# Optimization experiments

Hardware: AMD Instinct MI355X
Metric: run time of the kernel (lower is better)

The kernel has to match this reference:

```python
import jax, jax.numpy as jnp
from jax import lax
import numpy as np

S, B, HP, WP, CIN, CO, DS, DI, K = 6, 1, 37, 37, 1536, 256, 16, 512, 4
N = HP * WP          # 1369 patches (37x37 grid)
OH, OW = 148, 148
HID = max(S * CO // 4, S)  # 384, attention hidden


def setup_inputs() -> dict:
    key = jax.random.key(0)
    ks = iter(jax.random.split(key, 64))
    def nrm(shape, scale):
        return jax.random.normal(next(ks), shape, jnp.float32) * scale
    inp = {}
    inp["features"] = nrm((S, B, 1, N, CIN), 1.0)
    # AdaptiveFusionModule (global branch)
    inp["proj_w"] = nrm((S, CO, CIN), CIN ** -0.5)          # per-source 1x1 conv
    inp["attn_w1"] = nrm((S * CO, HID), (S * CO) ** -0.5)
    inp["attn_b1"] = jnp.zeros((HID,), jnp.float32)
    inp["attn_w2"] = nrm((HID, S), HID ** -0.5)
    inp["attn_b2"] = jnp.zeros((S,), jnp.float32)
    inp["src_scale"] = jnp.ones((S,), jnp.float32)
    # two SelectiveSSM parameter sets (fwd / bwd scan)
    def ssm_params(tag):
        d = {}
        d[tag + "_in_w"] = nrm((CO, 2 * DI), CO ** -0.5)
        d[tag + "_conv_w"] = nrm((K, DI), K ** -0.5)         # depthwise causal conv
        d[tag + "_conv_b"] = jnp.zeros((DI,), jnp.float32)
        d[tag + "_xp_w"] = nrm((DI, 2 * DS + DI + 1), 0.02)  # B, C, delta, dt_bias
        # trained A_log; scaled so the log-domain cumsum stays in fp32 range over L=1369
        d[tag + "_Alog"] = jnp.log(jnp.arange(1, DS + 1, dtype=jnp.float32) / 1000.0) * jnp.ones((DI, 1), jnp.float32)
        d[tag + "_D"] = jnp.ones((DI,), jnp.float32)
        d[tag + "_out_w"] = nrm((DI, CO), DI ** -0.5)
        d[tag + "_ln_g"] = jnp.ones((CO,), jnp.float32)
        d[tag + "_ln_b"] = jnp.zeros((CO,), jnp.float32)
        return d
    inp.update(ssm_params("f"))
    inp.update(ssm_params("b"))
    inp["merge_w"] = nrm((2 * CO, CO), (2 * CO) ** -0.5)     # MSSR merge 1x1 conv
    inp["co1_w"] = nrm((3, 3, CO, CO), (9 * CO) ** -0.5)     # conv_out1, HWIO
    inp["co1_b"] = jnp.zeros((CO,), jnp.float32)
    inp["hp"], inp["wp"], inp["out_h"], inp["out_w"] = HP, WP, OH, OW
    return inp


def _causal_dwconv(z, w, b):
    # z: [B,L,D], w: [K,D] -> torch Conv1d(groups=D, padding=K-1)[..., :L]
    Kk, L = w.shape[0], z.shape[1]
    zp = jnp.pad(z, ((0, 0), (Kk - 1, 0), (0, 0)))
    return sum(zp[:, k:k + L, :] * w[k] for k in range(Kk)) + b


def _ssm(x, in_w, conv_w, conv_b, xp_w, Alog, D, out_w, ln_g, ln_b):
    # x: [B,L,d_model] -> [B,L,d_model]
    z, gate = jnp.split(x @ in_w, 2, axis=-1)               # [B,L,DI] each
    z = jax.nn.silu(_causal_dwconv(z, conv_w, conv_b))
    xp = z @ xp_w                                           # [B,L,2*DS+DI+1]
    ds = Alog.shape[1]
    Bp, Cp = xp[..., :ds], xp[..., ds:2 * ds]
    delta = jax.nn.softplus(xp[..., 2 * ds:-1] + xp[..., -1:])  # [B,L,DI]
    dA = jnp.exp(delta[..., None] * (-jnp.exp(Alog)))       # [B,L,DI,DS]
    dBu = delta[..., None] * Bp[:, :, None, :] * z[..., None]
    # log-domain cumsum scan: h[t] = sum_s exp(cs[t]-cs[s]) * dBu[s]
    cs = jnp.cumsum(jnp.log(jnp.clip(dA, 1e-38)), axis=1)
    h = jnp.exp(cs) * jnp.cumsum(jnp.exp(-cs) * dBu, axis=1)
    y = (h * Cp[:, :, None, :]).sum(-1) + D * z             # [B,L,DI]
    y = (y * jax.nn.silu(gate)) @ out_w                     # [B,L,d_model]
    r = y + x                                               # residual + LayerNorm
    mu = r.mean(-1, keepdims=True)
    v = ((r - mu) ** 2).mean(-1, keepdims=True)
    return ln_g * (r - mu) * lax.rsqrt(v + 1e-5) + ln_b


def _forward(features, proj_w, attn_w1, attn_b1, attn_w2, attn_b2, src_scale,
             f_in_w, f_conv_w, f_conv_b, f_xp_w, f_Alog, f_D, f_out_w, f_ln_g, f_ln_b,
             b_in_w, b_conv_w, b_conv_b, b_xp_w, b_Alog, b_D, b_out_w, b_ln_g, b_ln_b,
             merge_w, co1_w, co1_b, hp, wp, out_h, out_w):
    feats = features[:, :, 0]                               # [S,B,N,Cin]
    pf = jnp.einsum('sbnc,soc->sbno', feats, proj_w)        # [S,B,N,Co] per-source 1x1 proj
    Bsz = pf.shape[1]
    concat = pf.mean(2).transpose(1, 0, 2).reshape(Bsz, -1)  # [B,S*Co] pooled concat
    w = jax.nn.softmax(jax.nn.relu(concat @ attn_w1 + attn_b1) @ attn_w2 + attn_b2, axis=-1)
    w = jax.nn.softmax(w * src_scale, axis=-1)              # double softmax as in torch
    fused = jnp.einsum('bs,sbnc->bnc', w, pf)               # [B,N,Co]
    # MSSR bidirectional scan over row-major flattened patches
    fwd = _ssm(fused, f_in_w, f_conv_w, f_conv_b, f_xp_w, f_Alog, f_D, f_out_w, f_ln_g, f_ln_b)
    bwd = _ssm(fused[:, ::-1], b_in_w, b_conv_w, b_conv_b, b_xp_w, b_Alog, b_D, b_out_w, b_ln_g, b_ln_b)[:, ::-1]
    out = jnp.concatenate([fwd, bwd], axis=-1) @ merge_w    # [B,N,Co]
    sp = out.reshape(Bsz, hp, wp, -1)                       # NHWC
    up = jax.image.resize(sp, (Bsz, out_h, out_w, sp.shape[-1]), method='bilinear')
    y = lax.conv_general_dilated(up, co1_w, (1, 1), 'SAME',
                                 dimension_numbers=('NHWC', 'HWIO', 'NHWC')) + co1_b
    return y.transpose(0, 3, 1, 2)                          # [B,Co,out_h,out_w]


def reference(features, proj_w, attn_w1, attn_b1, attn_w2, attn_b2, src_scale,
              f_in_w, f_conv_w, f_conv_b, f_xp_w, f_Alog, f_D, f_out_w, f_ln_g, f_ln_b,
              b_in_w, b_conv_w, b_conv_b, b_xp_w, b_Alog, b_D, b_out_w, b_ln_g, b_ln_b,
              merge_w, co1_w, co1_b, hp, wp, out_h, out_w):
    return _forward(features, proj_w, attn_w1, attn_b1, attn_w2, attn_b2, src_scale,
                    f_in_w, f_conv_w, f_conv_b, f_xp_w, f_Alog, f_D, f_out_w, f_ln_g, f_ln_b,
                    b_in_w, b_conv_w, b_conv_b, b_xp_w, b_Alog, b_D, b_out_w, b_ln_g, b_ln_b,
                    merge_w, co1_w, co1_b, hp, wp, out_h, out_w)
```

## Files before the change

kernel.cpp:

```cpp
#include <hip/hip_runtime.h>
#include <math.h>


namespace {
constexpr int kS   = 6;
constexpr int kHP  = 37;
constexpr int kWP  = 37;
constexpr int kN   = 1369;
constexpr int kCIN = 1536;
constexpr int kCO  = 256;
constexpr int kDS  = 16;
constexpr int kDI  = 512;
constexpr int kHID = 384;
constexpr int kOH  = 148;
constexpr int kOW  = 148;
constexpr int kNP  = kOH * kOW;
constexpr int kXPW = 545;
constexpr long kXPS = 746112;
constexpr int kNC  = 24;
constexpr int kCH  = 58;

constexpr long OFF_PF      = 0;
constexpr long OFF_Z2B     = 0;
constexpr long OFF_YGB     = 0;
constexpr long OFF_UPB     = 0;
constexpr long OFF_SCANP   = 700928;
constexpr long OFF_SCANH   = 1094144;
constexpr long OFF_HIN     = 1487360;
constexpr long OFF_OUTWT   = 1880576;
constexpr long OFF_COLPART = 2102784;
constexpr long OFF_WFIN    = 2119680;
constexpr long OFF_ATTNP   = 2119696;
constexpr long OFF_INWT    = 2200000;
constexpr long OFF_FUSEDB  = 2462144;
constexpr long OFF_ZG      = 2820624;
constexpr long OFF_Z       = 5760000;
constexpr long OFF_WCONVB  = 6000000;
constexpr long OFF_XP      = 7161856;
constexpr long OFF_DELTA   = 8654080;
constexpr long OFF_Y       = 10055936;
constexpr long OFF_GT      = 11457792;
constexpr long OFF_XPWT    = 11457792;
constexpr long OFF_FUSED2  = 12158720;
constexpr long OFF_CAT     = 12859648;
constexpr long OFF_MERGEWT = 13210112;
constexpr long OFF_MERGED  = 13560576;
}

typedef __attribute__((ext_vector_type(8))) short bf16x8;
typedef __attribute__((ext_vector_type(4))) float f32x4;

__device__ __forceinline__ short f2bf(float x) {
    unsigned u = __builtin_bit_cast(unsigned, x);
    unsigned r = u + 0x7fffu + ((u >> 16) & 1u);
    return (short)(r >> 16);
}

__device__ __forceinline__ bf16x8 cvt8(float4 x, float4 y) {
    union { short s[8]; bf16x8 v; } u;
    u.s[0] = f2bf(x.x); u.s[1] = f2bf(x.y); u.s[2] = f2bf(x.z); u.s[3] = f2bf(x.w);
    u.s[4] = f2bf(y.x); u.s[5] = f2bf(y.y); u.s[6] = f2bf(y.z); u.s[7] = f2bf(y.w);
    return u.v;
}

__global__ __launch_bounds__(256)
void transpose_cast_kernel(const float* __restrict__ w0, const float* __restrict__ w1,
                           short* __restrict__ wt, int K, int N)
{
    __shared__ float tile[32][33];
    int dir = blockIdx.z;
    const float* w = dir ? w1 : w0;
    short* o = wt + (long)dir * K * N;
    int k0 = blockIdx.x * 32, n0 = blockIdx.y * 32;
    int tx = threadIdx.x & 31, ty = threadIdx.x >> 5;
    #pragma unroll
    for (int r = 0; r < 32; r += 8) {
        int k = k0 + ty + r, n = n0 + tx;
        tile[ty + r][tx] = (k < K && n < N) ? w[(long)k * N + n] : 0.f;
    }
    __syncthreads();
    #pragma unroll
    for (int r = 0; r < 32; r += 8) {
        int n = n0 + ty + r, k = k0 + tx;
        if (n < N && k < K) o[(long)n * K + k] = f2bf(tile[tx][ty + r]);
    }
}

__global__ __launch_bounds__(256)
void mfma_nt(const short* __restrict__ A, long sA,
             const short* __restrict__ B, long sB,
             float* __restrict__ C, long sC,
             int M, int N, int K)
{
    __shared__ short smem[2][4096];
    const int bz = blockIdx.z;
    const short* Ab = A + (long)bz * sA;
    const short* Bb = B + (long)bz * sB;
    float* Cb = C + (long)bz * sC;
    const int t = threadIdx.x, w = t >> 6, l = t & 63;
    const int lr = l & 15, sg = l >> 4;
    const int m0 = blockIdx.x * 64, n0 = blockIdx.y * 64;

    const int row = t >> 2, qa = t & 3;
    int am = m0 + row; if (am >= M) am = M - 1;
    int bn = n0 + row; if (bn >= N) bn = N - 1;
    const long ga = (long)am * K + qa * 8;
    const long gb = (long)bn * K + qa * 8;
    const int woffA = row * 64 + ((qa ^ ((row >> 1) & 3)) << 4);
    const int woffB = 4096 + woffA;

    int aoff[2], boff[2];
    #pragma unroll
    for (int mi = 0; mi < 2; ++mi) {
        int r = (w >> 1) * 32 + mi * 16 + lr;
        aoff[mi] = r * 64 + ((sg ^ ((r >> 1) & 3)) << 4);
    }
    #pragma unroll
    for (int ni = 0; ni < 2; ++ni) {
        int r = (w & 1) * 32 + ni * 16 + lr;
        boff[ni] = 4096 + r * 64 + ((sg ^ ((r >> 1) & 3)) << 4);
    }

    f32x4 acc[2][2] = {};
    const int NT = K >> 5;
    {
        bf16x8 sa = *(const bf16x8*)(Ab + ga);
        bf16x8 sb = *(const bf16x8*)(Bb + gb);
        char* lb = (char*)&smem[0][0];
        *(bf16x8*)(lb + woffA) = sa;
        *(bf16x8*)(lb + woffB) = sb;
    }
    __syncthreads();
    for (int tt = 0; tt < NT; ++tt) {
        bf16x8 nsa, nsb;
        if (tt + 1 < NT) {
            long o = (long)(tt + 1) * 32;
            nsa = *(const bf16x8*)(Ab + ga + o);
            nsb = *(const bf16x8*)(Bb + gb + o);
        }
        char* lb = (char*)&smem[tt & 1][0];
        bf16x8 a[2], b[2];
        #pragma unroll
        for (int mi = 0; mi < 2; ++mi) a[mi] = *(const bf16x8*)(lb + aoff[mi]);
        #pragma unroll
        for (int ni = 0; ni < 2; ++ni) b[ni] = *(const bf16x8*)(lb + boff[ni]);
        #pragma unroll
        for (int mi = 0; mi < 2; ++mi)
            #pragma unroll
            for (int ni = 0; ni < 2; ++ni)
                acc[mi][ni] = __builtin_amdgcn_mfma_f32_16x16x32_bf16(a[mi], b[ni], acc[mi][ni], 0, 0, 0);
        if (tt + 1 < NT) {
            char* nb = (char*)&smem[(tt + 1) & 1][0];
            *(bf16x8*)(nb + woffA) = nsa;
            *(bf16x8*)(nb + woffB) = nsb;
        }
        __syncthreads();
    }
    const int q = l >> 4;
    const int wm0 = m0 + (w >> 1) * 32, wn0 = n0 + (w & 1) * 32;
    #pragma unroll
    for (int mi = 0; mi < 2; ++mi)
        #pragma unroll
        for (int ni = 0; ni < 2; ++ni)
            #pragma unroll
            for (int r = 0; r < 4; ++r) {
                int m = wm0 + mi * 16 + q * 4 + r;
                int n = wn0 + ni * 16 + lr;
                if (m < M && n < N)
                    Cb[(long)m * N + n] = acc[mi][ni][r];
            }
}

__global__ __launch_bounds__(256)
void proj_mfma_kernel(const float* __restrict__ Af, const float* __restrict__ Bf,
                      float* __restrict__ pf)
{
    __shared__ short smem[2][10240];
    const int bid = blockIdx.x;
    const int xcd = bid & 7, slot = bid >> 3;
    const int wid = (xcd < 4) ? xcd * 17 + slot : 68 + (xcd - 4) * 16 + slot;
    const int s = wid / 22, mblk = wid - s * 22;
    const float* A = Af + (long)s * kN * kCIN;
    const float* B = Bf + (long)s * kCO * kCIN;
    float* C = pf + (long)s * kN * kCO;
    const int m0 = mblk * 64;

    const int t = threadIdx.x, w = t >> 6, l = t & 63;
    const int lr = l & 15, sg = l >> 4;

    const int row = t >> 2, qa = t & 3;
    int am = m0 + row; if (am >= kN) am = kN - 1;
    const long ga = (long)am * kCIN + qa * 8;
    const int woffA = row * 64 + ((qa ^ ((row >> 1) & 3)) << 4);
    long gb[4]; int woffB[4];
    #pragma unroll
    for (int j = 0; j < 4; ++j) {
        int br = row + j * 64;
        gb[j] = (long)br * kCIN + qa * 8;
        woffB[j] = 4096 + br * 64 + ((qa ^ ((br >> 1) & 3)) << 4);
    }

    int aoff[4], boff[4];
    #pragma unroll
    for (int mi = 0; mi < 4; ++mi) {
        int r = mi * 16 + lr;
        aoff[mi] = r * 64 + ((sg ^ ((r >> 1) & 3)) << 4);
    }
    #pragma unroll
    for (int ni = 0; ni < 4; ++ni) {
        int r = w * 64 + ni * 16 + lr;
        boff[ni] = 4096 + r * 64 + ((sg ^ ((r >> 1) & 3)) << 4);
    }

    f32x4 acc[4][4] = {};
    const int NT = kCIN >> 5;
    {
        char* lb = (char*)&smem[0][0];
        float4 a0 = *(const float4*)(A + ga), a1 = *(const float4*)(A + ga + 4);
        *(bf16x8*)(lb + woffA) = cvt8(a0, a1);
        #pragma unroll
        for (int j = 0; j < 4; ++j) {
            float4 b0 = *(const float4*)(B + gb[j]), b1 = *(const float4*)(B + gb[j] + 4);
            *(bf16x8*)(lb + woffB[j]) = cvt8(b0, b1);
        }
    }
    __syncthreads();
    for (int tt = 0; tt < NT; ++tt) {
        float4 na0, na1, nb0[4], nb1[4];
        if (tt + 1 < NT) {
            long o = (long)(tt + 1) * 32;
            na0 = *(const float4*)(A + ga + o);
            na1 = *(const float4*)(A + ga + o + 4);
            #pragma unroll
            for (int j = 0; j < 4; ++j) {
                nb0[j] = *(const float4*)(B + gb[j] + o);
                nb1[j] = *(const float4*)(B + gb[j] + o + 4);
            }
        }
        char* lb = (char*)&smem[tt & 1][0];
        bf16x8 a[4], b[4];
        #pragma unroll
        for (int mi = 0; mi < 4; ++mi) a[mi] = *(const bf16x8*)(lb + aoff[mi]);
        #pragma unroll
        for (int ni = 0; ni < 4; ++ni) b[ni] = *(const bf16x8*)(lb + boff[ni]);
        #pragma unroll
        for (int mi = 0; mi < 4; ++mi)
            #pragma unroll
            for (int ni = 0; ni < 4; ++ni)
                acc[mi][ni] = __builtin_amdgcn_mfma_f32_16x16x32_bf16(a[mi], b[ni], acc[mi][ni], 0, 0, 0);
        if (tt + 1 < NT) {
            char* nb = (char*)&smem[(tt + 1) & 1][0];
            *(bf16x8*)(nb + woffA) = cvt8(na0, na1);
            #pragma unroll
            for (int j = 0; j < 4; ++j)
                *(bf16x8*)(nb + woffB[j]) = cvt8(nb0[j], nb1[j]);
        }
        __syncthreads();
    }
    const int q = l >> 4;
    const int wn0 = w * 64;
    #pragma unroll
    for (int mi = 0; mi < 4; ++mi)
        #pragma unroll
        for (int ni = 0; ni < 4; ++ni)
            #pragma unroll
            for (int r = 0; r < 4; ++r) {
                int m = m0 + mi * 16 + q * 4 + r;
                if (m < kN)
                    C[(long)m * kCO + wn0 + ni * 16 + lr] = acc[mi][ni][r];
            }
}

__global__ __launch_bounds__(256)
void conv_mfma_kernel(const short* __restrict__ up, const short* __restrict__ wt,
                      const float* __restrict__ bias, float* __restrict__ out)
{
    __shared__ short smem[2][12288];
    const int t = threadIdx.x, w = t >> 6, l = t & 63;
    const int lr = l & 15, sg = l >> 4;
    const int pm0 = blockIdx.x * 64;
    const int bn0 = blockIdx.y * 128;

    const int srow = t >> 3, qa = t & 7;
    long gA[2]; int woffA[2];
    #pragma unroll
    for (int j = 0; j < 2; ++j) {
        int ar = srow + j * 32;
        int p = pm0 + ar; if (p >= kNP) p = kNP - 1;
        int oy = p / kOW, ox = p - oy * kOW;
        gA[j] = ((long)oy * 150 + ox) * kCO + qa * 8;
        woffA[j] = ar * 128 + ((qa ^ (ar & 7)) << 4);
    }
    long gB[4]; int woffB[4];
    #pragma unroll
    for (int j = 0; j < 4; ++j) {
        int br = srow + j * 32;
        gB[j] = (long)(bn0 + br) * 2304 + qa * 8;
        woffB[j] = 8192 + br * 128 + ((qa ^ (br & 7)) << 4);
    }

    int aoff[2][2], boff[4][2];
    #pragma unroll
    for (int mi = 0; mi < 2; ++mi) {
        int r = (w >> 1) * 32 + mi * 16 + lr;
        #pragma unroll
        for (int kk = 0; kk < 2; ++kk)
            aoff[mi][kk] = r * 128 + (((kk * 4 + sg) ^ (r & 7)) << 4);
    }
    #pragma unroll
    for (int ni = 0; ni < 4; ++ni) {
        int r = (w & 1) * 64 + ni * 16 + lr;
        #pragma unroll
        for (int kk = 0; kk < 2; ++kk)
            boff[ni][kk] = 8192 + r * 128 + (((kk * 4 + sg) ^ (r & 7)) << 4);
    }

    f32x4 acc[2][4] = {};
    const int NT = 36;
    {
        char* lb = (char*)&smem[0][0];
        #pragma unroll
        for (int j = 0; j < 2; ++j)
            *(bf16x8*)(lb + woffA[j]) = *(const bf16x8*)(up + gA[j]);
        #pragma unroll
        for (int j = 0; j < 4; ++j)
            *(bf16x8*)(lb + woffB[j]) = *(const bf16x8*)(wt + gB[j]);
    }
    __syncthreads();

    for (int tt = 0; tt < NT; ++tt) {
        bf16x8 sa[2], sb[4];
        if (tt + 1 < NT) {
            int tn = tt + 1;
            int tap = tn >> 2, c0 = (tn & 3) << 6;
            int ky = tap / 3, kx = tap - ky * 3;
            long ta = ((long)ky * 150 + kx) * kCO + c0;
            long tb = (long)tn * 64;
            #pragma unroll
            for (int j = 0; j < 2; ++j) sa[j] = *(const bf16x8*)(up + gA[j] + ta);
            #pragma unroll
            for (int j = 0; j < 4; ++j) sb[j] = *(const bf16x8*)(wt + gB[j] + tb);
        }
        char* lb = (char*)&smem[tt & 1][0];
        #pragma unroll
        for (int kk = 0; kk < 2; ++kk) {
            bf16x8 a[2], b[4];
            #pragma unroll
            for (int mi = 0; mi < 2; ++mi) a[mi] = *(const bf16x8*)(lb + aoff[mi][kk]);
            #pragma unroll
            for (int ni = 0; ni < 4; ++ni) b[ni] = *(const bf16x8*)(lb + boff[ni][kk]);
            #pragma unroll
            for (int mi = 0; mi < 2; ++mi)
                #pragma unroll
                for (int ni = 0; ni < 4; ++ni)
                    acc[mi][ni] = __builtin_amdgcn_mfma_f32_16x16x32_bf16(a[mi], b[ni], acc[mi][ni], 0, 0, 0);
        }
        if (tt + 1 < NT) {
            char* nb = (char*)&smem[(tt + 1) & 1][0];
            #pragma unroll
            for (int j = 0; j < 2; ++j) *(bf16x8*)(nb + woffA[j]) = sa[j];
            #pragma unroll
            for (int j = 0; j < 4; ++j) *(bf16x8*)(nb + woffB[j]) = sb[j];
        }
        __syncthreads();
    }

    const int q = l >> 4;
    const int m0 = pm0 + (w >> 1) * 32;
    const int n0 = bn0 + (w & 1) * 64;
    #pragma unroll
    for (int mi = 0; mi < 2; ++mi)
        #pragma unroll
        for (int ni = 0; ni < 4; ++ni) {
            const int co = n0 + ni * 16 + lr;
            const float bv = bias[co];
            #pragma unroll
            for (int r = 0; r < 4; ++r) {
                int p = m0 + mi * 16 + q * 4 + r;
                if (p < kNP)
                    out[(long)co * kNP + p] = acc[mi][ni][r] + bv;
            }
        }
}

__global__ __launch_bounds__(256)
void colmean_kernel(const float* __restrict__ pf, float* __restrict__ colpart)
{
    int s = blockIdx.x, ch = blockIdx.y, o = threadIdx.x;
    int n0 = ch * 128, n1 = n0 + 128 > kN ? kN : n0 + 128;
    float a = 0.f;
    for (int n = n0; n < n1; ++n) a += pf[((long)s * kN + n) * kCO + o];
    colpart[ch * kS * kCO + s * kCO + o] = a;
}

__global__ __launch_bounds__(384)
void attn_part1(const float* __restrict__ colpart, const float* __restrict__ w1,
                float* __restrict__ partial)
{
    __shared__ float cm[128];
    int b = blockIdx.x, t = threadIdx.x;
    int c0 = b * 128;
    if (t < 128) {
        float a = 0.f;
        #pragma unroll
        for (int ch = 0; ch < 11; ++ch) a += colpart[ch * kS * kCO + c0 + t];
        cm[t] = a * (1.f / kN);
    }
    __syncthreads();
    float acc = 0.f;
    #pragma unroll 4
    for (int c = 0; c < 128; ++c) acc += cm[c] * w1[(long)(c0 + c) * kHID + t];
    partial[b * kHID + t] = acc;
}

__global__ __launch_bounds__(384)
void attn_part2(const float* __restrict__ partial, const float* __restrict__ b1,
                const float* __restrict__ w2, const float* __restrict__ b2,
                const float* __restrict__ ss, float* __restrict__ wfin)
{
    __shared__ float h[kHID];
    __shared__ float logits[8];
    int t = threadIdx.x;
    float acc = b1[t];
    #pragma unroll
    for (int b = 0; b < 12; ++b) acc += partial[b * kHID + t];
    h[t] = fmaxf(acc, 0.f);
    __syncthreads();
    if (t < kS) {
        float lg = b2[t];
        for (int j = 0; j < kHID; ++j) lg += h[j] * w2[j * kS + t];
        logits[t] = lg;
    }
    __syncthreads();
    if (t == 0) {
        float w[kS], mx = -1e30f, sum = 0.f;
        for (int s = 0; s < kS; ++s) mx = fmaxf(mx, logits[s]);
        for (int s = 0; s < kS; ++s) { w[s] = expf(logits[s] - mx); sum += w[s]; }
        for (int s = 0; s < kS; ++s) w[s] /= sum;
        mx = -1e30f;
        for (int s = 0; s < kS; ++s) { w[s] *= ss[s]; mx = fmaxf(mx, w[s]); }
        sum = 0.f;
        float e[kS];
        for (int s = 0; s < kS; ++s) { e[s] = expf(w[s] - mx); sum += e[s]; }
        for (int s = 0; s < kS; ++s) wfin[s] = e[s] / sum;
    }
}

__global__ __launch_bounds__(256)
void fuse_kernel(const float* __restrict__ pf, const float* __restrict__ wfin,
                 float* __restrict__ fused2, short* __restrict__ fusedb2)
{
    long idx = (long)blockIdx.x * 256 + threadIdx.x;
    if (idx >= (long)kN * kCO) return;
    float acc = 0.f;
    #pragma unroll
    for (int s = 0; s < kS; ++s) acc += wfin[s] * pf[(long)s * kN * kCO + idx];
    long n = idx / kCO; int c = (int)(idx % kCO);
    long ridx = (long)kN * kCO + (kN - 1 - n) * kCO + c;
    short bv = f2bf(acc);
    fused2[idx] = acc;
    fused2[ridx] = acc;
    fusedb2[idx] = bv;
    fusedb2[ridx] = bv;
}

__global__ __launch_bounds__(256)
void dwconv_kernel(const float* __restrict__ zg2,
                   const float* __restrict__ wf, const float* __restrict__ bf,
                   const float* __restrict__ wb, const float* __restrict__ bb,
                   float* __restrict__ z2, short* __restrict__ z2b)
{
    long idx = (long)blockIdx.x * 256 + threadIdx.x;
    int dir = blockIdx.y;
    if (idx >= (long)kN * kDI) return;
    long n = idx >> 9; int i = (int)(idx & (kDI - 1));
    const float* zg = zg2 + (long)dir * kN * 2 * kDI;
    const float* w  = dir ? wb : wf;
    const float* b  = dir ? bb : bf;
    float acc = b[i];
    #pragma unroll
    for (int k = 0; k < 4; ++k) {
        long m = n - 3 + k;
        if (m >= 0) acc += w[k * kDI + i] * zg[m * 2 * kDI + i];
    }
    float sg = 1.f / (1.f + expf(-acc));
    float v = acc * sg;
    z2 [(long)dir * kN * kDI + idx] = v;
    z2b[(long)dir * kN * kDI + idx] = f2bf(v);
}

__global__ __launch_bounds__(256)
void delta_kernel(const float* __restrict__ xp2, float* __restrict__ delta2)
{
    long idx = (long)blockIdx.x * 256 + threadIdx.x;
    int dir = blockIdx.y;
    if (idx >= (long)kN * kDI) return;
    long n = idx >> 9; int i = (int)(idx & (kDI - 1));
    const float* xp = xp2 + (long)dir * kXPS + n * kXPW;
    float x = xp[2 * kDS + i] + xp[kXPW - 1];
    float sp = fmaxf(x, 0.f) + log1pf(expf(-fabsf(x)));
    delta2[(long)dir * kN * kDI + idx] = sp;
}

__global__ __launch_bounds__(256)
void scan_partA(const float* __restrict__ delta2, const float* __restrict__ z2,
                const float* __restrict__ xp2,
                const float* __restrict__ Alogf, const float* __restrict__ Alogb,
                float* __restrict__ chunkP, float* __restrict__ chunkH)
{
    int bx = blockIdx.x;
    int c  = blockIdx.y;
    int dir = bx >> 5, iblk = bx & 31;
    int t = threadIdx.x;
    int s = t & 15, il = t >> 4;
    int i = iblk * 16 + il;
    int gid = dir * 8192 + iblk * 256 + t;
    const float* delta = delta2 + (long)dir * kN * kDI;
    const float* z     = z2     + (long)dir * kN * kDI;
    const float* xp    = xp2    + (long)dir * kXPS;
    const float* Alog  = dir ? Alogb : Alogf;
    float A = expf(Alog[i * kDS + s]);
    int n0 = c * kCH, n1 = n0 + kCH; if (n1 > kN) n1 = kN;
    float h = 0.f, P = 1.f;
    for (int n = n0; n < n1; ++n) {
        float dlt = delta[(long)n * kDI + i];
        float zv  = z[(long)n * kDI + i];
        float Bv  = xp[(long)n * kXPW + s];
        float dA  = __expf(-dlt * A);
        h = dA * h + dlt * Bv * zv;
        P *= dA;
    }
    chunkP[(long)c * 16384 + gid] = P;
    chunkH[(long)c * 16384 + gid] = h;
}

__global__ __launch_bounds__(256)
void scan_partB(const float* __restrict__ chunkP, const float* __restrict__ chunkH,
                float* __restrict__ hin)
{
    int gid = blockIdx.x * 256 + threadIdx.x;
    float H = 0.f;
    for (int c = 0; c < kNC; ++c) {
        hin[(long)c * 16384 + gid] = H;
        H = chunkP[(long)c * 16384 + gid] * H + chunkH[(long)c * 16384 + gid];
    }
}

__global__ __launch_bounds__(256)
void scan_partC(const float* __restrict__ delta2, const float* __restrict__ z2,
                const float* __restrict__ xp2,
                const float* __restrict__ Df, const float* __restrict__ Db,
                const float* __restrict__ Alogf, const float* __restrict__ Alogb,
                const float* __restrict__ hin, float* __restrict__ ybuf2)
{
    int bx = blockIdx.x;
    int c  = blockIdx.y;
    int dir = bx >> 5, iblk = bx & 31;
    int t = threadIdx.x;
    int s = t & 15, il = t >> 4;
    int i = iblk * 16 + il;
    int gid = dir * 8192 + iblk * 256 + t;
    const float* delta = delta2 + (long)dir * kN * kDI;
    const float* z     = z2     + (long)dir * kN * kDI;
    const float* xp    = xp2    + (long)dir * kXPS;
    const float* D     = dir ? Db : Df;
    const float* Alog  = dir ? Alogb : Alogf;
    float* y           = ybuf2  + (long)dir * kN * kDI;
    float A  = expf(Alog[i * kDS + s]);
    float Dv = D[i];
    int n0 = c * kCH, n1 = n0 + kCH; if (n1 > kN) n1 = kN;
    float h = hin[(long)c * 16384 + gid];
    for (int n = n0; n < n1; ++n) {
        float dlt = delta[(long)n * kDI + i];
        float zv  = z[(long)n * kDI + i];
        float Bv  = xp[(long)n * kXPW + s];
        float Cv  = xp[(long)n * kXPW + kDS + s];
        float dA  = __expf(-dlt * A);
        h = dA * h + dlt * Bv * zv;
        float cc = h * Cv;
        cc += __shfl_xor(cc, 1, 16);
        cc += __shfl_xor(cc, 2, 16);
        cc += __shfl_xor(cc, 4, 16);
        cc += __shfl_xor(cc, 8, 16);
        if (s == 0) y[(long)n * kDI + i] = cc + Dv * zv;
    }
}

__global__ __launch_bounds__(256)
void mulgate_kernel(const float* __restrict__ zg2, const float* __restrict__ ybuf2,
                    short* __restrict__ ygb)
{
    long idx = (long)blockIdx.x * 256 + threadIdx.x;
    int dir = blockIdx.y;
    if (idx >= (long)kN * kDI) return;
    long n = idx >> 9; int i = (int)(idx & (kDI - 1));
    float g = zg2[(long)dir * kN * 2 * kDI + n * 2 * kDI + kDI + i];
    float sg = 1.f / (1.f + expf(-g));
    float v = ybuf2[(long)dir * kN * kDI + idx] * g * sg;
    ygb[(long)dir * kN * kDI + idx] = f2bf(v);
}

__global__ __launch_bounds__(256)
void resid_ln_cat_kernel(const float* __restrict__ gt2, const float* __restrict__ x2,
                         const float* __restrict__ gf, const float* __restrict__ betf,
                         const float* __restrict__ gb, const float* __restrict__ betb,
                         short* __restrict__ catb)
{
    int n = blockIdx.x, dir = blockIdx.y, t = threadIdx.x;
    const float* gt = gt2 + ((long)dir * kN + n) * kCO;
    const float* x  = x2  + ((long)dir * kN + n) * kCO;
    const float* g  = dir ? gb : gf;
    const float* be = dir ? betb : betf;
    float r = gt[t] + x[t];
    float s1 = r, s2 = r * r;
    #pragma unroll
    for (int m = 32; m >= 1; m >>= 1) {
        s1 += __shfl_xor(s1, m, 64);
        s2 += __shfl_xor(s2, m, 64);
    }
    __shared__ float red[8];
    int w = t >> 6;
    if ((t & 63) == 0) { red[w] = s1; red[4 + w] = s2; }
    __syncthreads();
    float S1 = red[0] + red[1] + red[2] + red[3];
    float S2 = red[4] + red[5] + red[6] + red[7];
    float mu  = S1 * (1.f / kCO);
    float var = S2 * (1.f / kCO) - mu * mu;
    float inv = rsqrtf(var + 1e-5f);
    float v = g[t] * (r - mu) * inv + be[t];
    int row = dir ? (kN - 1 - n) : n;
    catb[(long)row * (2 * kCO) + dir * kCO + t] = f2bf(v);
}

__global__ __launch_bounds__(256)
void upsample_kernel(const float* __restrict__ merged, short* __restrict__ up)
{
    int p = blockIdx.x;
    int oy = p / kOW, ox = p - oy * kOW;
    int c = threadIdx.x;
    float sy = (oy + 0.5f) * ((float)kHP / (float)kOH) - 0.5f;
    float sx = (ox + 0.5f) * ((float)kWP / (float)kOW) - 0.5f;
    int iy0 = (int)floorf(sy); float fy = sy - (float)iy0;
    int ix0 = (int)floorf(sx); float fx = sx - (float)ix0;
    float wy0 = 1.f - fy, wy1 = fy, wx0 = 1.f - fx, wx1 = fx;
    int iy1 = iy0 + 1, ix1 = ix0 + 1;
    if (iy0 < 0)       { iy0 = 0;       wy0 = 0.f; }
    if (iy1 > kHP - 1) { iy1 = kHP - 1; wy1 = 0.f; }
    if (ix0 < 0)       { ix0 = 0;       wx0 = 0.f; }
    if (ix1 > kWP - 1) { ix1 = kWP - 1; wx1 = 0.f; }
    float wys = wy0 + wy1; wy0 /= wys; wy1 /= wys;
    float wxs = wx0 + wx1; wx0 /= wxs; wx1 /= wxs;
    const float* M00 = merged + (long)(iy0 * kWP + ix0) * kCO;
    const float* M01 = merged + (long)(iy0 * kWP + ix1) * kCO;
    const float* M10 = merged + (long)(iy1 * kWP + ix0) * kCO;
    const float* M11 = merged + (long)(iy1 * kWP + ix1) * kCO;
    float v = wy0 * (wx0 * M00[c] + wx1 * M01[c]) + wy1 * (wx0 * M10[c] + wx1 * M11[c]);
    up[((long)(oy + 1) * 150 + (ox + 1)) * kCO + c] = f2bf(v);
}

extern "C" void kernel_launch(void* const* d_in, const int* in_sizes, int n_in,
                              void* d_out, int out_size, void* d_ws, size_t ws_size,
                              hipStream_t stream)
{
    (void)in_sizes; (void)n_in; (void)out_size; (void)ws_size;
    const float* features  = (const float*)d_in[0];
    const float* proj_w    = (const float*)d_in[1];
    const float* attn_w1   = (const float*)d_in[2];
    const float* attn_b1   = (const float*)d_in[3];
    const float* attn_w2   = (const float*)d_in[4];
    const float* attn_b2   = (const float*)d_in[5];
    const float* src_scale = (const float*)d_in[6];
    const float* f_in_w    = (const float*)d_in[7];
    const float* f_conv_w  = (const float*)d_in[8];
    const float* f_conv_b  = (const float*)d_in[9];
    const float* f_xp_w    = (const float*)d_in[10];
    const float* f_Alog    = (const float*)d_in[11];
    const float* f_D       = (const float*)d_in[12];
    const float* f_out_w   = (const float*)d_in[13];
    const float* f_ln_g    = (const float*)d_in[14];
    const float* f_ln_b    = (const float*)d_in[15];
    const float* b_in_w    = (const float*)d_in[16];
    const float* b_conv_w  = (const float*)d_in[17];
    const float* b_conv_b  = (const float*)d_in[18];
    const float* b_xp_w    = (const float*)d_in[19];
    const float* b_Alog    = (const float*)d_in[20];
    const float* b_D       = (const float*)d_in[21];
    const float* b_out_w   = (const float*)d_in[22];
    const float* b_ln_g    = (const float*)d_in[23];
    const float* b_ln_b    = (const float*)d_in[24];
    const float* merge_w   = (const float*)d_in[25];
    const float* co1_w     = (const float*)d_in[26];
    const float* co1_b     = (const float*)d_in[27];

    float* ws      = (float*)d_ws;
    float* outp    = (float*)d_out;
    float* pf      = ws + OFF_PF;
    float* colpart = ws + OFF_COLPART;
    float* wfin    = ws + OFF_WFIN;
    float* attnp   = ws + OFF_ATTNP;
    float* fused2  = ws + OFF_FUSED2;
    float* zg2     = ws + OFF_ZG;
    float* z2      = ws + OFF_Z;
    float* xp2     = ws + OFF_XP;
    float* delta2  = ws + OFF_DELTA;
    float* ybuf2   = ws + OFF_Y;
    float* gt2     = ws + OFF_GT;
    float* merged  = ws + OFF_MERGED;
    float* chunkP  = ws + OFF_SCANP;
    float* chunkH  = ws + OFF_SCANH;
    float* hin     = ws + OFF_HIN;
    short* in_wt   = (short*)(ws + OFF_INWT);
    short* xp_wt   = (short*)(ws + OFF_XPWT);
    short* out_wt  = (short*)(ws + OFF_OUTWT);
    short* mrg_wt  = (short*)(ws + OFF_MERGEWT);
    short* fusedb2 = (short*)(ws + OFF_FUSEDB);
    short* z2b     = (short*)(ws + OFF_Z2B);
    short* ygb     = (short*)(ws + OFF_YGB);
    short* catb    = (short*)(ws + OFF_CAT);
    short* upb     = (short*)(ws + OFF_UPB);
    short* wconvb  = (short*)(ws + OFF_WCONVB);

    proj_mfma_kernel<<<dim3(132), 256, 0, stream>>>(features, proj_w, pf);
    transpose_cast_kernel<<<dim3(8, 32, 2), 256, 0, stream>>>(f_in_w, b_in_w, in_wt, 256, 1024);
    transpose_cast_kernel<<<dim3(16, 18, 2), 256, 0, stream>>>(f_xp_w, b_xp_w, xp_wt, 512, 545);
    transpose_cast_kernel<<<dim3(16, 8, 1), 256, 0, stream>>>(merge_w, merge_w, mrg_wt, 512, 256);
    colmean_kernel<<<dim3(6, 11), 256, 0, stream>>>(pf, colpart);
    attn_part1<<<dim3(12), 384, 0, stream>>>(colpart, attn_w1, attnp);
    attn_part2<<<1, 384, 0, stream>>>(attnp, attn_b1, attn_w2, attn_b2, src_scale, wfin);
    fuse_kernel<<<dim3(1369), 256, 0, stream>>>(pf, wfin, fused2, fusedb2);
    transpose_cast_kernel<<<dim3(16, 8, 2), 256, 0, stream>>>(f_out_w, b_out_w, out_wt, 512, 256);
    mfma_nt<<<dim3(22, 16, 2), 256, 0, stream>>>(
        fusedb2, (long)kN * kCO, in_wt, (long)2 * kDI * kCO,
        zg2, (long)kN * 2 * kDI, kN, 2 * kDI, kCO);
    dwconv_kernel<<<dim3(2738, 2), 256, 0, stream>>>(zg2, f_conv_w, f_conv_b,
                                                     b_conv_w, b_conv_b, z2, z2b);
    mfma_nt<<<dim3(22, 9, 2), 256, 0, stream>>>(
        z2b, (long)kN * kDI, xp_wt, (long)kXPW * kDI,
        xp2, kXPS, kN, kXPW, kDI);
    delta_kernel<<<dim3(2738, 2), 256, 0, stream>>>(xp2, delta2);
    scan_partA<<<dim3(64, kNC), 256, 0, stream>>>(delta2, z2, xp2, f_Alog, b_Alog,
                                                  chunkP, chunkH);
    scan_partB<<<dim3(64), 256, 0, stream>>>(chunkP, chunkH, hin);
    scan_partC<<<dim3(64, kNC), 256, 0, stream>>>(delta2, z2, xp2, f_D, b_D,
                                                  f_Alog, b_Alog, hin, ybuf2);
    mulgate_kernel<<<dim3(2738, 2), 256, 0, stream>>>(zg2, ybuf2, ygb);
    mfma_nt<<<dim3(22, 4, 2), 256, 0, stream>>>(
        ygb, (long)kN * kDI, out_wt, (long)kCO * kDI,
        gt2, (long)kN * kCO, kN, kCO, kDI);
    resid_ln_cat_kernel<<<dim3(1369, 2), 256, 0, stream>>>(gt2, fused2, f_ln_g, f_ln_b,
                                                           b_ln_g, b_ln_b, catb);
    mfma_nt<<<dim3(22, 4, 1), 256, 0, stream>>>(
        catb, 0, mrg_wt, 0,
        merged, 0, kN, kCO, 2 * kCO);
    transpose_cast_kernel<<<dim3(72, 8, 1), 256, 0, stream>>>(co1_w, co1_w, wconvb, 2304, 256);
    hipMemsetAsync(upb, 0, (size_t)150 * 150 * 256 * sizeof(short), stream);
    upsample_kernel<<<dim3(kNP), 256, 0, stream>>>(merged, upb);
    conv_mfma_kernel<<<dim3(343, 2), 256, 0, stream>>>(upb, wconvb, co1_b, outp);
}
```

Before: 310.9 us.

## Fuse delta softplus and gating into scan kernels; retile projection GEMM

Softplus delta computation moves into scan_partA and scan_partC, so the delta buffer is no longer written and re-read. The SiLU gating and bf16 cast are folded into the scan_partC epilogue, which removes the mulgate kernel and the fp32 y buffer. The projection GEMM changes from 132 blocks of 64x256 tiles with K-step 32 to a 22x2x6 grid of 64x128 tiles with K-step 64 and a new swizzle. The trade-off is that the softplus work is now done twice (once in each scan pass) and per-thread in every scan lane, and the projection grid loses its XCD-aware block mapping.

```diff
diff --git a/kernel.cpp b/kernel.cpp
--- a/kernel.cpp
+++ b/kernel.cpp
@@ -37,8 +37,6 @@
 constexpr long OFF_Z       = 5760000;
 constexpr long OFF_WCONVB  = 6000000;
 constexpr long OFF_XP      = 7161856;
-constexpr long OFF_DELTA   = 8654080;
-constexpr long OFF_Y       = 10055936;
 constexpr long OFF_GT      = 11457792;
 constexpr long OFF_XPWT    = 11457792;
 constexpr long OFF_FUSED2  = 12158720;
@@ -175,97 +173,113 @@
 void proj_mfma_kernel(const float* __restrict__ Af, const float* __restrict__ Bf,
                       float* __restrict__ pf)
 {
-    __shared__ short smem[2][10240];
-    const int bid = blockIdx.x;
-    const int xcd = bid & 7, slot = bid >> 3;
-    const int wid = (xcd < 4) ? xcd * 17 + slot : 68 + (xcd - 4) * 16 + slot;
-    const int s = wid / 22, mblk = wid - s * 22;
+    __shared__ short smem[2][12288];
+    const int s = blockIdx.z;
     const float* A = Af + (long)s * kN * kCIN;
     const float* B = Bf + (long)s * kCO * kCIN;
     float* C = pf + (long)s * kN * kCO;
-    const int m0 = mblk * 64;
-
+    const int m0 = blockIdx.x * 64, n0 = blockIdx.y * 128;
     const int t = threadIdx.x, w = t >> 6, l = t & 63;
     const int lr = l & 15, sg = l >> 4;
 
-    const int row = t >> 2, qa = t & 3;
-    int am = m0 + row; if (am >= kN) am = kN - 1;
-    const long ga = (long)am * kCIN + qa * 8;
-    const int woffA = row * 64 + ((qa ^ ((row >> 1) & 3)) << 4);
-    long gb[4]; int woffB[4];
+    const int srow = t >> 3, qa = t & 7;
+    long gA[2]; int woffA[2];
+    #pragma unroll
+    for (int j = 0; j < 2; ++j) {
+        int ar = srow + j * 32;
+        int am = m0 + ar; if (am >= kN) am = kN - 1;
+        gA[j] = (long)am * kCIN + qa * 8;
+        woffA[j] = ar * 128 + ((qa ^ (ar & 7)) << 4);
+    }
+    long gB[4]; int woffB[4];
     #pragma unroll
     for (int j = 0; j < 4; ++j) {
-        int br = row + j * 64;
-        gb[j] = (long)br * kCIN + qa * 8;
-        woffB[j] = 4096 + br * 64 + ((qa ^ ((br >> 1) & 3)) << 4);
-    }
-
-    int aoff[4], boff[4];
-    #pragma unroll
-    for (int mi = 0; mi < 4; ++mi) {
-        int r = mi * 16 + lr;
-        aoff[mi] = r * 64 + ((sg ^ ((r >> 1) & 3)) << 4);
+        int br = srow + j * 32;
+        gB[j] = (long)(n0 + br) * kCIN + qa * 8;
+        woffB[j] = 8192 + br * 128 + ((qa ^ (br & 7)) << 4);
+    }
+
+    int aoff[2][2], boff[4][2];
+    #pragma unroll
+    for (int mi = 0; mi < 2; ++mi) {
+        int r = (w >> 1) * 32 + mi * 16 + lr;
+        #pragma unroll
+        for (int kk = 0; kk < 2; ++kk)
+            aoff[mi][kk] = r * 128 + (((kk * 4 + sg) ^ (r & 7)) << 4);
     }
     #pragma unroll
     for (int ni = 0; ni < 4; ++ni) {
-        int r = w * 64 + ni * 16 + lr;
-        boff[ni] = 4096 + r * 64 + ((sg ^ ((r >> 1) & 3)) << 4);
-    }
-
-    f32x4 acc[4][4] = {};
-    const int NT = kCIN >> 5;
+        int r = (w & 1) * 64 + ni * 16 + lr;
+        #pragma unroll
+        for (int kk = 0; kk < 2; ++kk)
+            boff[ni][kk] = 8192 + r * 128 + (((kk * 4 + sg) ^ (r & 7)) << 4);
+    }
+
+    f32x4 acc[2][4] = {};
+    const int NT = kCIN >> 6;
     {
         char* lb = (char*)&smem[0][0];
-        float4 a0 = *(const float4*)(A + ga), a1 = *(const float4*)(A + ga + 4);
-        *(bf16x8*)(lb + woffA) = cvt8(a0, a1);
+        #pragma unroll
+        for (int j = 0; j < 2; ++j) {
+            float4 x = *(const float4*)(A + gA[j]), y = *(const float4*)(A + gA[j] + 4);
+            *(bf16x8*)(lb + woffA[j]) = cvt8(x, y);
+        }
         #pragma unroll
         for (int j = 0; j < 4; ++j) {
-            float4 b0 = *(const float4*)(B + gb[j]), b1 = *(const float4*)(B + gb[j] + 4);
-            *(bf16x8*)(lb + woffB[j]) = cvt8(b0, b1);
+            float4 x = *(const float4*)(B + gB[j]), y = *(const float4*)(B + gB[j] + 4);
+            *(bf16x8*)(lb + woffB[j]) = cvt8(x, y);
         }
     }
     __syncthreads();
+
     for (int tt = 0; tt < NT; ++tt) {
-        float4 na0, na1, nb0[4], nb1[4];
+        float4 na0[2], na1[2], nb0[4], nb1[4];
         if (tt + 1 < NT) {
-            long o = (long)(tt + 1) * 32;
-            na0 = *(const float4*)(A + ga + o);
-            na1 = *(const float4*)(A + ga + o + 4);
+            long o = (long)(tt + 1) * 64;
+            #pragma unroll
+            for (int j = 0; j < 2; ++j) {
+                na0[j] = *(const float4*)(A + gA[j] + o);
+                na1[j] = *(const float4*)(A + gA[j] + o + 4);
+            }
             #pragma unroll
             for (int j = 0; j < 4; ++j) {
-                nb0[j] = *(const float4*)(B + gb[j] + o);
-                nb1[j] = *(const float4*)(B + gb[j] + o + 4);
+                nb0[j] = *(const float4*)(B + gB[j] + o);
+                nb1[j] = *(const float4*)(B + gB[j] + o + 4);
             }
         }
         char* lb = (char*)&smem[tt & 1][0];
-        bf16x8 a[4], b[4];
-        #pragma unroll
-        for (int mi = 0; mi < 4; ++mi) a[mi] = *(const bf16x8*)(lb + aoff[mi]);
-        #pragma unroll
-        for (int ni = 0; ni < 4; ++ni) b[ni] = *(const bf16x8*)(lb + boff[ni]);
-        #pragma unroll
-        for (int mi = 0; mi < 4; ++mi)
-            #pragma unroll
-            for (int ni = 0; ni < 4; ++ni)
-                acc[mi][ni] = __builtin_amdgcn_mfma_f32_16x16x32_bf16(a[mi], b[ni], acc[mi][ni], 0, 0, 0);
+        #pragma unroll
+        for (int kk = 0; kk < 2; ++kk) {
+            bf16x8 a[2], b[4];
+            #pragma unroll
+            for (int mi = 0; mi < 2; ++mi) a[mi] = *(const bf16x8*)(lb + aoff[mi][kk]);
+            #pragma unroll
+            for (int ni = 0; ni < 4; ++ni) b[ni] = *(const bf16x8*)(lb + boff[ni][kk]);
+            #pragma unroll
+            for (int mi = 0; mi < 2; ++mi)
+                #pragma unroll
+                for (int ni = 0; ni < 4; ++ni)
+                    acc[mi][ni] = __builtin_amdgcn_mfma_f32_16x16x32_bf16(a[mi], b[ni], acc[mi][ni], 0, 0, 0);
+        }
         if (tt + 1 < NT) {
             char* nb = (char*)&smem[(tt + 1) & 1][0];
-            *(bf16x8*)(nb + woffA) = cvt8(na0, na1);
-            #pragma unroll
-            for (int j = 0; j < 4; ++j)
-                *(bf16x8*)(nb + woffB[j]) = cvt8(nb0[j], nb1[j]);
+            #pragma unroll
+            for (int j = 0; j < 2; ++j) *(bf16x8*)(nb + woffA[j]) = cvt8(na0[j], na1[j]);
+            #pragma unroll
+            for (int j = 0; j < 4; ++j) *(bf16x8*)(nb + woffB[j]) = cvt8(nb0[j], nb1[j]);
         }
         __syncthreads();
     }
+
     const int q = l >> 4;
-    const int wn0 = w * 64;
-    #pragma unroll
-    for (int mi = 0; mi < 4; ++mi)
+    const int wm0 = m0 + (w >> 1) * 32, wn0 = n0 + (w & 1) * 64;
+    #pragma unroll
+    for (int mi = 0; mi < 2; ++mi)
         #pragma unroll
         for (int ni = 0; ni < 4; ++ni)
             #pragma unroll
             for (int r = 0; r < 4; ++r) {
-                int m = m0 + mi * 16 + q * 4 + r;
+                int m = wm0 + mi * 16 + q * 4 + r;
                 if (m < kN)
                     C[(long)m * kCO + wn0 + ni * 16 + lr] = acc[mi][ni][r];
             }
@@ -490,21 +504,7 @@
 }
 
 __global__ __launch_bounds__(256)
-void delta_kernel(const float* __restrict__ xp2, float* __restrict__ delta2)
-{
-    long idx = (long)blockIdx.x * 256 + threadIdx.x;
-    int dir = blockIdx.y;
-    if (idx >= (long)kN * kDI) return;
-    long n = idx >> 9; int i = (int)(idx & (kDI - 1));
-    const float* xp = xp2 + (long)dir * kXPS + n * kXPW;
-    float x = xp[2 * kDS + i] + xp[kXPW - 1];
-    float sp = fmaxf(x, 0.f) + log1pf(expf(-fabsf(x)));
-    delta2[(long)dir * kN * kDI + idx] = sp;
-}
-
-__global__ __launch_bounds__(256)
-void scan_partA(const float* __restrict__ delta2, const float* __restrict__ z2,
-                const float* __restrict__ xp2,
+void scan_partA(const float* __restrict__ z2, const float* __restrict__ xp2,
                 const float* __restrict__ Alogf, const float* __restrict__ Alogb,
                 float* __restrict__ chunkP, float* __restrict__ chunkH)
 {
@@ -515,7 +515,6 @@
     int s = t & 15, il = t >> 4;
     int i = iblk * 16 + il;
     int gid = dir * 8192 + iblk * 256 + t;
-    const float* delta = delta2 + (long)dir * kN * kDI;
     const float* z     = z2     + (long)dir * kN * kDI;
     const float* xp    = xp2    + (long)dir * kXPS;
     const float* Alog  = dir ? Alogb : Alogf;
@@ -523,9 +522,11 @@
     int n0 = c * kCH, n1 = n0 + kCH; if (n1 > kN) n1 = kN;
     float h = 0.f, P = 1.f;
     for (int n = n0; n < n1; ++n) {
-        float dlt = delta[(long)n * kDI + i];
+        const float* xr = xp + (long)n * kXPW;
         float zv  = z[(long)n * kDI + i];
-        float Bv  = xp[(long)n * kXPW + s];
+        float Bv  = xr[s];
+        float x   = xr[2 * kDS + i] + xr[kXPW - 1];
+        float dlt = fmaxf(x, 0.f) + log1pf(expf(-fabsf(x)));
         float dA  = __expf(-dlt * A);
         h = dA * h + dlt * Bv * zv;
         P *= dA;
@@ -547,11 +548,11 @@
 }
 
 __global__ __launch_bounds__(256)
-void scan_partC(const float* __restrict__ delta2, const float* __restrict__ z2,
-                const float* __restrict__ xp2,
+void scan_partC(const float* __restrict__ z2, const float* __restrict__ xp2,
+                const float* __restrict__ zg2,
                 const float* __restrict__ Df, const float* __restrict__ Db,
                 const float* __restrict__ Alogf, const float* __restrict__ Alogb,
-                const float* __restrict__ hin, float* __restrict__ ybuf2)
+                const float* __restrict__ hin, short* __restrict__ ygb)
 {
     int bx = blockIdx.x;
     int c  = blockIdx.y;
@@ -560,21 +561,23 @@
     int s = t & 15, il = t >> 4;
     int i = iblk * 16 + il;
     int gid = dir * 8192 + iblk * 256 + t;
-    const float* delta = delta2 + (long)dir * kN * kDI;
     const float* z     = z2     + (long)dir * kN * kDI;
     const float* xp    = xp2    + (long)dir * kXPS;
+    const float* zg    = zg2    + (long)dir * kN * 2 * kDI;
     const float* D     = dir ? Db : Df;
     const float* Alog  = dir ? Alogb : Alogf;
-    float* y           = ybuf2  + (long)dir * kN * kDI;
+    short* y           = ygb    + (long)dir * kN * kDI;
     float A  = expf(Alog[i * kDS + s]);
     float Dv = D[i];
     int n0 = c * kCH, n1 = n0 + kCH; if (n1 > kN) n1 = kN;
     float h = hin[(long)c * 16384 + gid];
     for (int n = n0; n < n1; ++n) {
-        float dlt = delta[(long)n * kDI + i];
+        const float* xr = xp + (long)n * kXPW;
         float zv  = z[(long)n * kDI + i];
-        float Bv  = xp[(long)n * kXPW + s];
-        float Cv  = xp[(long)n * kXPW + kDS + s];
+        float Bv  = xr[s];
+        float Cv  = xr[kDS + s];
+        float x   = xr[2 * kDS + i] + xr[kXPW - 1];
+        float dlt = fmaxf(x, 0.f) + log1pf(expf(-fabsf(x)));
         float dA  = __expf(-dlt * A);
         h = dA * h + dlt * Bv * zv;
         float cc = h * Cv;
@@ -582,22 +585,13 @@
         cc += __shfl_xor(cc, 2, 16);
         cc += __shfl_xor(cc, 4, 16);
         cc += __shfl_xor(cc, 8, 16);
-        if (s == 0) y[(long)n * kDI + i] = cc + Dv * zv;
-    }
-}
-
-__global__ __launch_bounds__(256)
-void mulgate_kernel(const float* __restrict__ zg2, const float* __restrict__ ybuf2,
-                    short* __restrict__ ygb)
-{
-    long idx = (long)blockIdx.x * 256 + threadIdx.x;
-    int dir = blockIdx.y;
-    if (idx >= (long)kN * kDI) return;
-    long n = idx >> 9; int i = (int)(idx & (kDI - 1));
-    float g = zg2[(long)dir * kN * 2 * kDI + n * 2 * kDI + kDI + i];
-    float sg = 1.f / (1.f + expf(-g));
-    float v = ybuf2[(long)dir * kN * kDI + idx] * g * sg;
-    ygb[(long)dir * kN * kDI + idx] = f2bf(v);
+        if (s == 0) {
+            float g = zg[(long)n * 2 * kDI + kDI + i];
+            float sgm = 1.f / (1.f + expf(-g));
+            float v = (cc + Dv * zv) * g * sgm;
+            y[(long)n * kDI + i] = f2bf(v);
+        }
+    }
 }
 
 __global__ __launch_bounds__(256)
@@ -702,8 +696,6 @@
     float* zg2     = ws + OFF_ZG;
     float* z2      = ws + OFF_Z;
     float* xp2     = ws + OFF_XP;
-    float* delta2  = ws + OFF_DELTA;
-    float* ybuf2   = ws + OFF_Y;
     float* gt2     = ws + OFF_GT;
     float* merged  = ws + OFF_MERGED;
     float* chunkP  = ws + OFF_SCANP;
@@ -720,7 +712,7 @@
     short* upb     = (short*)(ws + OFF_UPB);
     short* wconvb  = (short*)(ws + OFF_WCONVB);
 
-    proj_mfma_kernel<<<dim3(132), 256, 0, stream>>>(features, proj_w, pf);
+    proj_mfma_kernel<<<dim3(22, 2, 6), 256, 0, stream>>>(features, proj_w, pf);
     transpose_cast_kernel<<<dim3(8, 32, 2), 256, 0, stream>>>(f_in_w, b_in_w, in_wt, 256, 1024);
     transpose_cast_kernel<<<dim3(16, 18, 2), 256, 0, stream>>>(f_xp_w, b_xp_w, xp_wt, 512, 545);
     transpose_cast_kernel<<<dim3(16, 8, 1), 256, 0, stream>>>(merge_w, merge_w, mrg_wt, 512, 256);
@@ -737,13 +729,11 @@
     mfma_nt<<<dim3(22, 9, 2), 256, 0, stream>>>(
         z2b, (long)kN * kDI, xp_wt, (long)kXPW * kDI,
         xp2, kXPS, kN, kXPW, kDI);
-    delta_kernel<<<dim3(2738, 2), 256, 0, stream>>>(xp2, delta2);
-    scan_partA<<<dim3(64, kNC), 256, 0, stream>>>(delta2, z2, xp2, f_Alog, b_Alog,
+    scan_partA<<<dim3(64, kNC), 256, 0, stream>>>(z2, xp2, f_Alog, b_Alog,
                                                   chunkP, chunkH);
     scan_partB<<<dim3(64), 256, 0, stream>>>(chunkP, chunkH, hin);
-    scan_partC<<<dim3(64, kNC), 256, 0, stream>>>(delta2, z2, xp2, f_D, b_D,
-                                                  f_Alog, b_Alog, hin, ybuf2);
-    mulgate_kernel<<<dim3(2738, 2), 256, 0, stream>>>(zg2, ybuf2, ygb);
+    scan_partC<<<dim3(64, kNC), 256, 0, stream>>>(z2, xp2, zg2, f_D, b_D,
+                                                  f_Alog, b_Alog, hin, ygb);
     mfma_nt<<<dim3(22, 4, 2), 256, 0, stream>>>(
         ygb, (long)kN * kDI, out_wt, (long)kCO * kDI,
         gt2, (long)kN * kCO, kN, kCO, kDI);
```

Result: slower. 452.3 us (+45.5%).
